# Performance work log

Hardware: AMD Instinct MI355X
Metric: run time of the kernel (lower is better)

## Reference

```python
import jax, jax.numpy as jnp
import numpy as np

EPS = 1e-6
GROUPS = 8


def setup_inputs() -> dict:
    key = jax.random.key(0)
    ks = jax.random.split(key, 8)
    B, C, H, W = 4, 128, 64, 64
    s = 1.0 / np.sqrt(C)
    return {
        "x": jax.random.normal(ks[0], (B, C, H, W), jnp.float32),
        "gn_scale": jnp.ones((C,), jnp.float32),
        "gn_bias": jnp.zeros((C,), jnp.float32),
        "wq": jax.random.normal(ks[1], (C, C), jnp.float32) * s,
        "bq": jnp.zeros((C,), jnp.float32),
        "wk": jax.random.normal(ks[2], (C, C), jnp.float32) * s,
        "bk": jnp.zeros((C,), jnp.float32),
        "wv": jax.random.normal(ks[3], (C, C), jnp.float32) * s,
        "bv": jnp.zeros((C,), jnp.float32),
        "wp": jax.random.normal(ks[4], (C, C), jnp.float32) * s,
        "bp": jnp.zeros((C,), jnp.float32),
    }


def _group_norm(x, scale, bias):
    B, C, H, W = x.shape
    g = x.reshape(B, GROUPS, C // GROUPS, H * W)
    mu = g.mean(axis=(2, 3), keepdims=True)
    var = g.var(axis=(2, 3), keepdims=True)
    g = (g - mu) * jax.lax.rsqrt(var + EPS)
    g = g.reshape(B, C, H, W)
    return g * scale[None, :, None, None] + bias[None, :, None, None]


def reference(x, gn_scale, gn_bias, wq, bq, wk, bk, wv, bv, wp, bp):
    B, C, H, W = x.shape
    N = H * W
    h = _group_norm(x, gn_scale, gn_bias).reshape(B, C, N)
    # 1x1 convs == channel matmuls: (C_out, C_in) x (B, C_in, N)
    q = jnp.einsum('oc,bcn->bon', wq, h) + bq[None, :, None]
    k = jnp.einsum('oc,bcn->bon', wk, h) + bk[None, :, None]
    v = jnp.einsum('oc,bcn->bon', wv, h) + bv[None, :, None]
    # scores: (B, N, N), w[b,n,m] = sum_c q[b,c,n] k[b,c,m]
    w = jnp.einsum('bcn,bcm->bnm', q, k) * (C ** -0.5)
    w = jax.nn.softmax(w, axis=-1)
    # h_[b,c,n] = sum_m w[b,n,m] v[b,c,m]
    h_ = jnp.einsum('bnm,bcm->bcn', w, v)
    out = jnp.einsum('oc,bcn->bon', wp, h_) + bp[None, :, None]
    return x + out.reshape(B, C, H, W)
```

## Files before the change

### kernel.cpp

```cpp
#include <hip/hip_runtime.h>
#include <math.h>

#define B_ 4
#define C_ 128
#define N_ 4096
#define NSPLIT 4
#define MT 32
#define PLD 40
#define HLD 136
#define VTLD 40

typedef float floatx4 __attribute__((ext_vector_type(4)));
typedef short bf16x8 __attribute__((ext_vector_type(8)));

__device__ __forceinline__ ushort f2bf(float f) {
  unsigned u = __float_as_uint(f);
  return (ushort)((u + 0x7FFF + ((u >> 16) & 1)) >> 16);
}
__device__ __forceinline__ float bf2f(ushort u) {
  return __uint_as_float(((unsigned)u) << 16);
}
__device__ __forceinline__ unsigned pkbf(float a, float b) {
  return __builtin_amdgcn_perm(__float_as_uint(a) + 0x8000u,
                               __float_as_uint(b) + 0x8000u, 0x07060302u);
}
__device__ __forceinline__ float fexp2(float x) {
#if __has_builtin(__builtin_amdgcn_exp2f)
  return __builtin_amdgcn_exp2f(x);
#else
  return exp2f(x);
#endif
}
__device__ __forceinline__ void gl2lds16(const ushort* g, ushort* l) {
  __builtin_amdgcn_global_load_lds(
      (const __attribute__((address_space(1))) void*)g,
      (__attribute__((address_space(3))) void*)l, 16, 0, 0);
}

__global__ __launch_bounds__(256) void prep_kernel(
    const float* __restrict__ x, float* __restrict__ gstat,
    const float* __restrict__ wq, const float* __restrict__ wk,
    const float* __restrict__ wv, const float* __restrict__ wp,
    ushort* __restrict__ wB) {
  if (blockIdx.x >= 256) {
    int i = (blockIdx.x - 256) * 256 + threadIdx.x;
    int m = i >> 14, j = i & 16383;
    const float* src = (m == 0) ? wq : (m == 1) ? wk : (m == 2) ? wv : wp;
    wB[i] = f2bf(src[j]);
    return;
  }
  int b = blockIdx.x >> 6, g = (blockIdx.x >> 3) & 7, part = blockIdx.x & 7;
  const float4* xp = (const float4*)(x + (size_t)(b * C_ + g * 16) * N_) + part * 2048;
  float s = 0.f, ss = 0.f;
  for (int i = threadIdx.x; i < 2048; i += 256) {
    float4 v = xp[i];
    s += v.x + v.y + v.z + v.w;
    ss += v.x * v.x + v.y * v.y + v.z * v.z + v.w * v.w;
  }
  #pragma unroll
  for (int o = 32; o > 0; o >>= 1) {
    s += __shfl_down(s, o, 64);
    ss += __shfl_down(ss, o, 64);
  }
  __shared__ float rs[4], rss[4];
  int wid = threadIdx.x >> 6, lane = threadIdx.x & 63;
  if (lane == 0) { rs[wid] = s; rss[wid] = ss; }
  __syncthreads();
  if (threadIdx.x == 0) {
    int slot = (b * 8 + g) * 8 + part;
    gstat[slot]       = rs[0] + rs[1] + rs[2] + rs[3];
    gstat[256 + slot] = rss[0] + rss[1] + rss[2] + rss[3];
  }
}

__global__ __launch_bounds__(256) void gnqkv_kernel(
    const float* __restrict__ x, const float* __restrict__ gstat,
    const float* __restrict__ scale, const float* __restrict__ bias,
    const ushort* __restrict__ wB,
    const float* __restrict__ bq, const float* __restrict__ bk,
    const float* __restrict__ bv,
    ushort* __restrict__ qT, ushort* __restrict__ kT, ushort* __restrict__ vB) {
  __shared__ __align__(16) ushort hs[32][HLD];
  __shared__ __align__(16) ushort Qt[32][HLD];
  __shared__ __align__(16) ushort Kt[32][HLD];
  __shared__ __align__(16) ushort Vt[128][VTLD];
  __shared__ float sSc[C_], sBi[C_];
  int tid = threadIdx.x;
  int b = blockIdx.x >> 7;
  int n0 = (blockIdx.x & 127) * 32;
  if (tid < 128) {
    int g = tid >> 4;
    float S = 0.f, SS = 0.f;
    #pragma unroll
    for (int p = 0; p < 8; ++p) {
      S  += gstat[(b * 8 + g) * 8 + p];
      SS += gstat[256 + (b * 8 + g) * 8 + p];
    }
    float mu = S * (1.f / 65536.f);
    float var = SS * (1.f / 65536.f) - mu * mu;
    float rstd = rsqrtf(var + 1e-6f);
    float sc = scale[tid] * rstd;
    sSc[tid] = sc;
    sBi[tid] = bias[tid] - mu * sc;
  }
  __syncthreads();
  #pragma unroll
  for (int k2 = 0; k2 < 4; ++k2) {
    int i = tid + k2 * 256;
    int c = i >> 3, n4 = i & 7;
    float4 v = *(const float4*)(x + (size_t)(b * C_ + c) * N_ + n0 + n4 * 4);
    float sc = sSc[c], bi = sBi[c];
    hs[n4 * 4 + 0][c] = f2bf(v.x * sc + bi);
    hs[n4 * 4 + 1][c] = f2bf(v.y * sc + bi);
    hs[n4 * 4 + 2][c] = f2bf(v.z * sc + bi);
    hs[n4 * 4 + 3][c] = f2bf(v.w * sc + bi);
  }
  __syncthreads();
  int lane = tid & 63, w = tid >> 6;
  int col = lane & 15, quad = lane >> 4;
  int oh = w * 32;
  bf16x8 hf[2][4];
  #pragma unroll
  for (int nh = 0; nh < 2; ++nh)
    #pragma unroll
    for (int kc = 0; kc < 4; ++kc)
      hf[nh][kc] = *(const bf16x8*)&hs[nh * 16 + col][kc * 32 + quad * 8];
  const ushort* Wq = wB;
  const ushort* Wk = wB + 16384;
  const ushort* Wv = wB + 32768;
  const float scl = 0.12751879752224991f;
  #pragma unroll
  for (int ot = 0; ot < 2; ++ot) {
    int o0 = oh + ot * 16;
    floatx4 aq[2] = {(floatx4)0.f, (floatx4)0.f};
    floatx4 ak[2] = {(floatx4)0.f, (floatx4)0.f};
    floatx4 av[2] = {(floatx4)0.f, (floatx4)0.f};
    #pragma unroll
    for (int kc = 0; kc < 4; ++kc) {
      int wo = (o0 + col) * C_ + kc * 32 + quad * 8;
      bf16x8 wqf = *(const bf16x8*)&Wq[wo];
      bf16x8 wkf = *(const bf16x8*)&Wk[wo];
      bf16x8 wvf = *(const bf16x8*)&Wv[wo];
      #pragma unroll
      for (int nh = 0; nh < 2; ++nh) {
        aq[nh] = __builtin_amdgcn_mfma_f32_16x16x32_bf16(wqf, hf[nh][kc], aq[nh], 0, 0, 0);
        ak[nh] = __builtin_amdgcn_mfma_f32_16x16x32_bf16(wkf, hf[nh][kc], ak[nh], 0, 0, 0);
        av[nh] = __builtin_amdgcn_mfma_f32_16x16x32_bf16(wvf, hf[nh][kc], av[nh], 0, 0, 0);
      }
    }
    float4 bqv = *(const float4*)&bq[o0 + quad * 4];
    float4 bkv = *(const float4*)&bk[o0 + quad * 4];
    float4 bvv = *(const float4*)&bv[o0 + quad * 4];
    #pragma unroll
    for (int nh = 0; nh < 2; ++nh) {
      uint2 qs = { pkbf((aq[nh][1] + bqv.y) * scl, (aq[nh][0] + bqv.x) * scl),
                   pkbf((aq[nh][3] + bqv.w) * scl, (aq[nh][2] + bqv.z) * scl) };
      uint2 ks = { pkbf(ak[nh][1] + bkv.y, ak[nh][0] + bkv.x),
                   pkbf(ak[nh][3] + bkv.w, ak[nh][2] + bkv.z) };
      *(uint2*)&Qt[nh * 16 + col][o0 + quad * 4] = qs;
      *(uint2*)&Kt[nh * 16 + col][o0 + quad * 4] = ks;
      float vv[4] = {av[nh][0] + bvv.x, av[nh][1] + bvv.y,
                     av[nh][2] + bvv.z, av[nh][3] + bvv.w};
      #pragma unroll
      for (int r = 0; r < 4; ++r)
        Vt[o0 + quad * 4 + r][nh * 16 + col] = f2bf(vv[r]);
    }
  }
  __syncthreads();
  #pragma unroll
  for (int rep = 0; rep < 2; ++rep) {
    int idx = tid + rep * 256;
    int row = idx >> 4, seg = idx & 15;
    size_t dst = ((size_t)b * N_ + n0 + row) * C_ + seg * 8;
    *(uint4*)(qT + dst) = *(const uint4*)&Qt[row][seg * 8];
    *(uint4*)(kT + dst) = *(const uint4*)&Kt[row][seg * 8];
  }
  #pragma unroll
  for (int rep = 0; rep < 2; ++rep) {
    int idx = tid + rep * 256;
    int o = idx >> 2, seg = idx & 3;
    *(uint4*)(vB + ((size_t)b * C_ + o) * N_ + n0 + seg * 8) = *(const uint4*)&Vt[o][seg * 8];
  }
}

__global__ __launch_bounds__(512, 4) void attn_kernel(
    const ushort* __restrict__ qT, const ushort* __restrict__ kT,
    const ushort* __restrict__ vB, ushort* __restrict__ Op,
    float* __restrict__ Lv) {
  __shared__ __align__(16) ushort Ks[2][MT * 128];
  __shared__ __align__(16) ushort Vs[2][C_ * MT];
  __shared__ __align__(16) ushort Ps[2][128 * PLD];
  __shared__ float lpart[8][2][16];
  int sp = blockIdx.x & 3;
  int qblk = (blockIdx.x >> 2) & 31;
  int b = blockIdx.x >> 7;
  int n0 = qblk * 128;
  int tid = threadIdx.x, lane = tid & 63, w = tid >> 6;
  int col = lane & 15, quad = lane >> 4;
  int wu = __builtin_amdgcn_readfirstlane(w);
  int mtw = w & 1, qg = w >> 1;
  int qh = w & 1, cq = w >> 1;
  const ushort* kTb = kT + (size_t)b * N_ * C_;
  const ushort* vBb = vB + (size_t)b * C_ * N_;

  bf16x8 qf[2][4];
  #pragma unroll
  for (int qt = 0; qt < 2; ++qt)
    #pragma unroll
    for (int kc = 0; kc < 4; ++kc)
      qf[qt][kc] = *(const bf16x8*)(qT + ((size_t)b * N_ + n0 + qg * 32 + qt * 16 + col) * C_ + kc * 32 + quad * 8);

  floatx4 Oacc[4][2];
  #pragma unroll
  for (int qt = 0; qt < 4; ++qt)
    #pragma unroll
    for (int ct = 0; ct < 2; ++ct) Oacc[qt][ct] = (floatx4)0.f;
  float lacc[2] = {0.f, 0.f};

  const int m00 = sp * 1024;

  const ushort* kgp;
  const ushort* vgp;
  {
    int r = wu * 4 + (lane >> 4);
    int pos = (lane & 15) ^ (r & 7);
    kgp = kTb + (size_t)(m00 + r) * 128 + pos * 8;
    int c = wu * 16 + (lane >> 2);
    int mc = (lane & 3) ^ ((lane >> 3) & 3);
    vgp = vBb + (size_t)c * N_ + m00 + mc * 8;
  }

  #define STAGE(buf)                                   \
    {                                                  \
      gl2lds16(kgp, &Ks[buf][wu * 512]);               \
      gl2lds16(vgp, &Vs[buf][wu * 512]);               \
      kgp += MT * 128;                                 \
      vgp += MT;                                       \
    }

  #define S_COMPUTE(KsB, st)                                                          \
    {                                                                                 \
      int row = mtw * 16 + col;                                                       \
      bf16x8 kf[4];                                                                   \
      _Pragma("unroll")                                                               \
      for (int kc = 0; kc < 4; ++kc)                                                  \
        kf[kc] = *(const bf16x8*)&(KsB)[row * 128 + (((4 * kc + quad) ^ (col & 7)) * 8)]; \
      __builtin_amdgcn_s_setprio(1);                                                  \
      _Pragma("unroll")                                                               \
      for (int qt = 0; qt < 2; ++qt) {                                                \
        floatx4 acc = (floatx4)0.f;                                                   \
        _Pragma("unroll")                                                             \
        for (int kc = 0; kc < 4; ++kc)                                                \
          acc = __builtin_amdgcn_mfma_f32_16x16x32_bf16(kf[kc], qf[qt][kc], acc, 0, 0, 0); \
        st[qt] = acc;                                                                 \
      }                                                                               \
      __builtin_amdgcn_s_setprio(0);                                                  \
    }

  #define SOFTMAX_WRITE(PsB, st)                                                      \
    {                                                                                 \
      _Pragma("unroll")                                                               \
      for (int qt = 0; qt < 2; ++qt) {                                                \
        int prow = (qg * 32 + qt * 16 + col) * PLD + mtw * 16;                        \
        float p0 = fexp2(st[qt][0]);                                                  \
        float p1 = fexp2(st[qt][1]);                                                  \
        float p2 = fexp2(st[qt][2]);                                                  \
        float p3 = fexp2(st[qt][3]);                                                  \
        uint2 pk = { pkbf(p1, p0), pkbf(p3, p2) };                                    \
        *(uint2*)&(PsB)[prow + quad * 4] = pk;                                        \
        lacc[qt] += (p0 + p1) + (p2 + p3);                                            \
      }                                                                               \
    }

  #define V_LOAD(VsB, vfp)                                                            \
    {                                                                                 \
      _Pragma("unroll")                                                               \
      for (int ct = 0; ct < 2; ++ct)                                                  \
        vfp[ct] = *(const bf16x8*)&(VsB)[(cq * 32 + ct * 16 + col) * MT +             \
                                         ((quad ^ ((col >> 1) & 3)) * 8)];            \
    }

  #define PV_COMPUTE(PsB, vfp)                                                        \
    {                                                                                 \
      __builtin_amdgcn_s_setprio(1);                                                  \
      _Pragma("unroll")                                                               \
      for (int qt = 0; qt < 4; ++qt) {                                                \
        bf16x8 pf = *(const bf16x8*)&(PsB)[(qh * 64 + qt * 16 + col) * PLD + quad * 8]; \
        _Pragma("unroll")                                                             \
        for (int ct = 0; ct < 2; ++ct)                                                \
          Oacc[qt][ct] = __builtin_amdgcn_mfma_f32_16x16x32_bf16(pf, vfp[ct], Oacc[qt][ct], 0, 0, 0); \
      }                                                                               \
      __builtin_amdgcn_s_setprio(0);                                                  \
    }

  floatx4 st[2];
  bf16x8 vfp[2];

  STAGE(0);
  __syncthreads();

  STAGE(1);
  S_COMPUTE(Ks[0], st);
  SOFTMAX_WRITE(Ps[0], st);
  V_LOAD(Vs[0], vfp);
  __syncthreads();

  for (int t = 1; t < 31; ++t) {
    STAGE((t + 1) & 1);
    S_COMPUTE(Ks[t & 1], st);
    PV_COMPUTE(Ps[(t - 1) & 1], vfp);
    SOFTMAX_WRITE(Ps[t & 1], st);
    V_LOAD(Vs[t & 1], vfp);
    __syncthreads();
  }

  S_COMPUTE(Ks[1], st);
  PV_COMPUTE(Ps[0], vfp);
  SOFTMAX_WRITE(Ps[1], st);
  V_LOAD(Vs[1], vfp);
  __syncthreads();

  PV_COMPUTE(Ps[1], vfp);

  ushort* OpB = Op + (((size_t)sp * B_ + b) * N_ + n0) * C_;
  #pragma unroll
  for (int qt = 0; qt < 4; ++qt)
    #pragma unroll
    for (int ct = 0; ct < 2; ++ct)
      #pragma unroll
      for (int r = 0; r < 4; ++r)
        OpB[(size_t)(qh * 64 + qt * 16 + quad * 4 + r) * C_ + cq * 32 + ct * 16 + col] =
            f2bf(Oacc[qt][ct][r]);
  #pragma unroll
  for (int qt = 0; qt < 2; ++qt) {
    float lsum = lacc[qt];
    lsum += __shfl_xor(lsum, 16, 64);
    lsum += __shfl_xor(lsum, 32, 64);
    if (quad == 0) lpart[w][qt][col] = lsum;
  }
  __syncthreads();
  if ((w & 1) == 0 && quad == 0) {
    #pragma unroll
    for (int qt = 0; qt < 2; ++qt) {
      int idx = b * N_ + n0 + (w >> 1) * 32 + qt * 16 + col;
      Lv[(size_t)sp * (B_ * N_) + idx] = lpart[w][qt][col] + lpart[w + 1][qt][col];
    }
  }
}

__global__ __launch_bounds__(256) void mergeproj_kernel(
    const ushort* __restrict__ Op, const float* __restrict__ Lv,
    const ushort* __restrict__ wpB, const float* __restrict__ bp,
    const float* __restrict__ x, float* __restrict__ out) {
  __shared__ __align__(16) ushort tile[32 * HLD];
  int tid = threadIdx.x;
  int b = blockIdx.x >> 7;
  int n0 = (blockIdx.x & 127) * 32;
  #pragma unroll
  for (int rep = 0; rep < 2; ++rep) {
    int idx = tid + rep * 256;
    int n = idx >> 4, cc = idx & 15;
    int nIdx = b * N_ + n0 + n;
    float den = Lv[0 * (B_ * N_) + nIdx] + Lv[1 * (B_ * N_) + nIdx] +
                Lv[2 * (B_ * N_) + nIdx] + Lv[3 * (B_ * N_) + nIdx];
    float inv = 1.f / den;
    float o[8];
    #pragma unroll
    for (int j = 0; j < 8; ++j) o[j] = 0.f;
    #pragma unroll
    for (int sp = 0; sp < NSPLIT; ++sp) {
      uint4 d = *(const uint4*)&Op[((size_t)sp * (B_ * N_) + nIdx) * C_ + cc * 8];
      unsigned dd[4] = {d.x, d.y, d.z, d.w};
      #pragma unroll
      for (int j = 0; j < 4; ++j) {
        o[j * 2]     += bf2f((ushort)(dd[j] & 0xFFFF));
        o[j * 2 + 1] += bf2f((ushort)(dd[j] >> 16));
      }
    }
    uint4 res;
    res.x = pkbf(o[1] * inv, o[0] * inv);
    res.y = pkbf(o[3] * inv, o[2] * inv);
    res.z = pkbf(o[5] * inv, o[4] * inv);
    res.w = pkbf(o[7] * inv, o[6] * inv);
    *(uint4*)&tile[n * HLD + cc * 8] = res;
  }
  __syncthreads();
  int lane = tid & 63, w = tid >> 6;
  int col = lane & 15, quad = lane >> 4;
  int oh = w * 32;
  bf16x8 hf[2][4];
  #pragma unroll
  for (int nh = 0; nh < 2; ++nh)
    #pragma unroll
    for (int kc = 0; kc < 4; ++kc)
      hf[nh][kc] = *(const bf16x8*)&tile[(nh * 16 + col) * HLD + kc * 32 + quad * 8];
  #pragma unroll
  for (int ot = 0; ot < 2; ++ot) {
    int o0 = oh + ot * 16;
    floatx4 acc[2] = {(floatx4)0.f, (floatx4)0.f};
    #pragma unroll
    for (int kc = 0; kc < 4; ++kc) {
      int wo = (o0 + col) * C_ + kc * 32 + quad * 8;
      bf16x8 wf = *(const bf16x8*)&wpB[wo];
      #pragma unroll
      for (int nh = 0; nh < 2; ++nh)
        acc[nh] = __builtin_amdgcn_mfma_f32_16x16x32_bf16(wf, hf[nh][kc], acc[nh], 0, 0, 0);
    }
    float4 bpv = *(const float4*)&bp[o0 + quad * 4];
    float bb[4] = {bpv.x, bpv.y, bpv.z, bpv.w};
    #pragma unroll
    for (int nh = 0; nh < 2; ++nh)
      #pragma unroll
      for (int r = 0; r < 4; ++r) {
        size_t idx = ((size_t)b * C_ + o0 + quad * 4 + r) * N_ + n0 + nh * 16 + col;
        out[idx] = acc[nh][r] + bb[r] + x[idx];
      }
  }
}

extern "C" void kernel_launch(void* const* d_in, const int* in_sizes, int n_in,
                              void* d_out, int out_size, void* d_ws, size_t ws_size,
                              hipStream_t stream) {
  const float* x        = (const float*)d_in[0];
  const float* gn_scale = (const float*)d_in[1];
  const float* gn_bias  = (const float*)d_in[2];
  const float* wq = (const float*)d_in[3];
  const float* bq = (const float*)d_in[4];
  const float* wk = (const float*)d_in[5];
  const float* bk = (const float*)d_in[6];
  const float* wv = (const float*)d_in[7];
  const float* bv = (const float*)d_in[8];
  const float* wp = (const float*)d_in[9];
  const float* bp = (const float*)d_in[10];
  float* out = (float*)d_out;

  char* ws = (char*)d_ws;
  float*  Lv    = (float*)(ws + 262144);
  ushort* wB    = (ushort*)(ws + 524288);
  float*  gstat = (float*)(ws + 655360);
  ushort* qT    = (ushort*)(ws + (4u << 20));
  ushort* kT    = (ushort*)(ws + (8u << 20));
  ushort* vB    = (ushort*)(ws + (12u << 20));
  ushort* Op    = (ushort*)(ws + (16u << 20));
  ushort* wpB   = wB + 49152;

  prep_kernel<<<512, 256, 0, stream>>>(x, gstat, wq, wk, wv, wp, wB);
  gnqkv_kernel<<<512, 256, 0, stream>>>(x, gstat, gn_scale, gn_bias, wB, bq, bk, bv, qT, kT, vB);
  attn_kernel<<<512, 512, 0, stream>>>(qT, kT, vB, Op, Lv);
  mergeproj_kernel<<<512, 256, 0, stream>>>(Op, Lv, wpB, bp, x, out);
}
```

Baseline: 142.2 us.

## Fuse four kernels into one persistent kernel with software grid barriers

Merges the prep, groupnorm+QKV, attention and merge+projection kernels into a single 512-block launch of 512 threads. The stages are separated by an atomic-counter grid barrier, and the shared-memory buffers of each stage are aliased onto one raw shared array. This removes three kernel launch gaps and their tail effects, at the cost of a memset launch and spin-wait barriers. It relies on all 512 blocks being co-resident; if they are not, the kernel deadlocks.

```diff
diff --git a/kernel.cpp b/kernel.cpp
--- a/kernel.cpp
+++ b/kernel.cpp
@@ -9,6 +9,7 @@
 #define PLD 40
 #define HLD 136
 #define VTLD 40
+#define NBLK 512u
 
 typedef float floatx4 __attribute__((ext_vector_type(4)));
 typedef short bf16x8 __attribute__((ext_vector_type(8)));
@@ -37,101 +38,123 @@
       (__attribute__((address_space(3))) void*)l, 16, 0, 0);
 }
 
-__global__ __launch_bounds__(256) void prep_kernel(
-    const float* __restrict__ x, float* __restrict__ gstat,
-    const float* __restrict__ wq, const float* __restrict__ wk,
-    const float* __restrict__ wv, const float* __restrict__ wp,
-    ushort* __restrict__ wB) {
-  if (blockIdx.x >= 256) {
-    int i = (blockIdx.x - 256) * 256 + threadIdx.x;
-    int m = i >> 14, j = i & 16383;
-    const float* src = (m == 0) ? wq : (m == 1) ? wk : (m == 2) ? wv : wp;
-    wB[i] = f2bf(src[j]);
-    return;
-  }
-  int b = blockIdx.x >> 6, g = (blockIdx.x >> 3) & 7, part = blockIdx.x & 7;
-  const float4* xp = (const float4*)(x + (size_t)(b * C_ + g * 16) * N_) + part * 2048;
-  float s = 0.f, ss = 0.f;
-  for (int i = threadIdx.x; i < 2048; i += 256) {
-    float4 v = xp[i];
-    s += v.x + v.y + v.z + v.w;
-    ss += v.x * v.x + v.y * v.y + v.z * v.z + v.w * v.w;
-  }
-  #pragma unroll
-  for (int o = 32; o > 0; o >>= 1) {
-    s += __shfl_down(s, o, 64);
-    ss += __shfl_down(ss, o, 64);
-  }
-  __shared__ float rs[4], rss[4];
-  int wid = threadIdx.x >> 6, lane = threadIdx.x & 63;
-  if (lane == 0) { rs[wid] = s; rss[wid] = ss; }
+__device__ __forceinline__ void grid_bar(unsigned* bar) {
   __syncthreads();
   if (threadIdx.x == 0) {
-    int slot = (b * 8 + g) * 8 + part;
-    gstat[slot]       = rs[0] + rs[1] + rs[2] + rs[3];
-    gstat[256 + slot] = rss[0] + rss[1] + rss[2] + rss[3];
-  }
-}
-
-__global__ __launch_bounds__(256) void gnqkv_kernel(
-    const float* __restrict__ x, const float* __restrict__ gstat,
-    const float* __restrict__ scale, const float* __restrict__ bias,
-    const ushort* __restrict__ wB,
-    const float* __restrict__ bq, const float* __restrict__ bk,
-    const float* __restrict__ bv,
-    ushort* __restrict__ qT, ushort* __restrict__ kT, ushort* __restrict__ vB) {
-  __shared__ __align__(16) ushort hs[32][HLD];
-  __shared__ __align__(16) ushort Qt[32][HLD];
-  __shared__ __align__(16) ushort Kt[32][HLD];
-  __shared__ __align__(16) ushort Vt[128][VTLD];
-  __shared__ float sSc[C_], sBi[C_];
-  int tid = threadIdx.x;
-  int b = blockIdx.x >> 7;
-  int n0 = (blockIdx.x & 127) * 32;
-  if (tid < 128) {
-    int g = tid >> 4;
-    float S = 0.f, SS = 0.f;
-    #pragma unroll
-    for (int p = 0; p < 8; ++p) {
-      S  += gstat[(b * 8 + g) * 8 + p];
-      SS += gstat[256 + (b * 8 + g) * 8 + p];
-    }
-    float mu = S * (1.f / 65536.f);
-    float var = SS * (1.f / 65536.f) - mu * mu;
-    float rstd = rsqrtf(var + 1e-6f);
-    float sc = scale[tid] * rstd;
-    sSc[tid] = sc;
-    sBi[tid] = bias[tid] - mu * sc;
+    unsigned gen = __hip_atomic_load(&bar[1], __ATOMIC_RELAXED, __HIP_MEMORY_SCOPE_AGENT);
+    unsigned prev = __hip_atomic_fetch_add(&bar[0], 1u, __ATOMIC_ACQ_REL, __HIP_MEMORY_SCOPE_AGENT);
+    if (prev + 1u == NBLK) {
+      __hip_atomic_store(&bar[0], 0u, __ATOMIC_RELAXED, __HIP_MEMORY_SCOPE_AGENT);
+      __hip_atomic_fetch_add(&bar[1], 1u, __ATOMIC_RELEASE, __HIP_MEMORY_SCOPE_AGENT);
+    } else {
+      while (__hip_atomic_load(&bar[1], __ATOMIC_ACQUIRE, __HIP_MEMORY_SCOPE_AGENT) == gen)
+        __builtin_amdgcn_s_sleep(2);
+    }
   }
   __syncthreads();
-  #pragma unroll
-  for (int k2 = 0; k2 < 4; ++k2) {
-    int i = tid + k2 * 256;
-    int c = i >> 3, n4 = i & 7;
-    float4 v = *(const float4*)(x + (size_t)(b * C_ + c) * N_ + n0 + n4 * 4);
-    float sc = sSc[c], bi = sBi[c];
-    hs[n4 * 4 + 0][c] = f2bf(v.x * sc + bi);
-    hs[n4 * 4 + 1][c] = f2bf(v.y * sc + bi);
-    hs[n4 * 4 + 2][c] = f2bf(v.z * sc + bi);
-    hs[n4 * 4 + 3][c] = f2bf(v.w * sc + bi);
+}
+
+__global__ __launch_bounds__(512, 4) void fused_kernel(
+    const float* __restrict__ x, const float* __restrict__ gn_scale,
+    const float* __restrict__ gn_bias,
+    const float* __restrict__ wq, const float* __restrict__ bq,
+    const float* __restrict__ wk, const float* __restrict__ bk,
+    const float* __restrict__ wv, const float* __restrict__ bv,
+    const float* __restrict__ wp, const float* __restrict__ bp,
+    float* __restrict__ out, unsigned* __restrict__ bar,
+    float* __restrict__ Lv, ushort* __restrict__ wB,
+    float* __restrict__ gstat, ushort* __restrict__ qT, ushort* __restrict__ kT,
+    ushort* __restrict__ vB, ushort* __restrict__ Op) {
+  __shared__ __align__(16) char smem[54272];
+  ushort* sm_u = (ushort*)smem;
+  int bx = blockIdx.x;
+  int tid = threadIdx.x, lane = tid & 63, w = tid >> 6;
+  int col = lane & 15, quad = lane >> 4;
+
+  if (bx >= 256) {
+    if (tid < 256) {
+      int i = (bx - 256) * 256 + tid;
+      int m = i >> 14, j = i & 16383;
+      const float* src = (m == 0) ? wq : (m == 1) ? wk : (m == 2) ? wv : wp;
+      wB[i] = f2bf(src[j]);
+    }
+  } else {
+    int b = bx >> 6, g = (bx >> 3) & 7, part = bx & 7;
+    const float4* xp = (const float4*)(x + (size_t)(b * C_ + g * 16) * N_) + part * 2048;
+    float s = 0.f, ss = 0.f;
+    for (int i = tid; i < 2048; i += 512) {
+      float4 v = xp[i];
+      s += v.x + v.y + v.z + v.w;
+      ss += v.x * v.x + v.y * v.y + v.z * v.z + v.w * v.w;
+    }
+    #pragma unroll
+    for (int o = 32; o > 0; o >>= 1) {
+      s += __shfl_down(s, o, 64);
+      ss += __shfl_down(ss, o, 64);
+    }
+    float* rs = (float*)smem;
+    float* rss = (float*)smem + 8;
+    if (lane == 0) { rs[w] = s; rss[w] = ss; }
+    __syncthreads();
+    if (tid == 0) {
+      float S = 0.f, SS = 0.f;
+      #pragma unroll
+      for (int k = 0; k < 8; ++k) { S += rs[k]; SS += rss[k]; }
+      int slot = (b * 8 + g) * 8 + part;
+      gstat[slot]       = S;
+      gstat[256 + slot] = SS;
+    }
   }
-  __syncthreads();
-  int lane = tid & 63, w = tid >> 6;
-  int col = lane & 15, quad = lane >> 4;
-  int oh = w * 32;
-  bf16x8 hf[2][4];
-  #pragma unroll
-  for (int nh = 0; nh < 2; ++nh)
-    #pragma unroll
-    for (int kc = 0; kc < 4; ++kc)
-      hf[nh][kc] = *(const bf16x8*)&hs[nh * 16 + col][kc * 32 + quad * 8];
-  const ushort* Wq = wB;
-  const ushort* Wk = wB + 16384;
-  const ushort* Wv = wB + 32768;
-  const float scl = 0.12751879752224991f;
-  #pragma unroll
-  for (int ot = 0; ot < 2; ++ot) {
-    int o0 = oh + ot * 16;
+  grid_bar(bar);
+
+  {
+    ushort* hs = sm_u;
+    ushort* Qt = sm_u + 4352;
+    ushort* Kt = sm_u + 8704;
+    ushort* Vt = sm_u + 13056;
+    float* sSc = (float*)(smem + 36352);
+    float* sBi = (float*)(smem + 36864);
+    int b = bx >> 7;
+    int n0 = (bx & 127) * 32;
+    if (tid < 128) {
+      int g = tid >> 4;
+      float S = 0.f, SS = 0.f;
+      #pragma unroll
+      for (int p = 0; p < 8; ++p) {
+        S  += gstat[(b * 8 + g) * 8 + p];
+        SS += gstat[256 + (b * 8 + g) * 8 + p];
+      }
+      float mu = S * (1.f / 65536.f);
+      float var = SS * (1.f / 65536.f) - mu * mu;
+      float rstd = rsqrtf(var + 1e-6f);
+      float sc = gn_scale[tid] * rstd;
+      sSc[tid] = sc;
+      sBi[tid] = gn_bias[tid] - mu * sc;
+    }
+    __syncthreads();
+    #pragma unroll
+    for (int k2 = 0; k2 < 2; ++k2) {
+      int i = tid + k2 * 512;
+      int c = i >> 3, n4 = i & 7;
+      float4 v = *(const float4*)(x + (size_t)(b * C_ + c) * N_ + n0 + n4 * 4);
+      float sc = sSc[c], bi = sBi[c];
+      hs[(n4 * 4 + 0) * HLD + c] = f2bf(v.x * sc + bi);
+      hs[(n4 * 4 + 1) * HLD + c] = f2bf(v.y * sc + bi);
+      hs[(n4 * 4 + 2) * HLD + c] = f2bf(v.z * sc + bi);
+      hs[(n4 * 4 + 3) * HLD + c] = f2bf(v.w * sc + bi);
+    }
+    __syncthreads();
+    int o0 = w * 16;
+    bf16x8 hf[2][4];
+    #pragma unroll
+    for (int nh = 0; nh < 2; ++nh)
+      #pragma unroll
+      for (int kc = 0; kc < 4; ++kc)
+        hf[nh][kc] = *(const bf16x8*)&hs[(nh * 16 + col) * HLD + kc * 32 + quad * 8];
+    const ushort* Wq = wB;
+    const ushort* Wk = wB + 16384;
+    const ushort* Wv = wB + 32768;
+    const float scl = 0.12751879752224991f;
     floatx4 aq[2] = {(floatx4)0.f, (floatx4)0.f};
     floatx4 ak[2] = {(floatx4)0.f, (floatx4)0.f};
     floatx4 av[2] = {(floatx4)0.f, (floatx4)0.f};
@@ -157,246 +180,229 @@
                    pkbf((aq[nh][3] + bqv.w) * scl, (aq[nh][2] + bqv.z) * scl) };
       uint2 ks = { pkbf(ak[nh][1] + bkv.y, ak[nh][0] + bkv.x),
                    pkbf(ak[nh][3] + bkv.w, ak[nh][2] + bkv.z) };
-      *(uint2*)&Qt[nh * 16 + col][o0 + quad * 4] = qs;
-      *(uint2*)&Kt[nh * 16 + col][o0 + quad * 4] = ks;
+      *(uint2*)&Qt[(nh * 16 + col) * HLD + o0 + quad * 4] = qs;
+      *(uint2*)&Kt[(nh * 16 + col) * HLD + o0 + quad * 4] = ks;
       float vv[4] = {av[nh][0] + bvv.x, av[nh][1] + bvv.y,
                      av[nh][2] + bvv.z, av[nh][3] + bvv.w};
       #pragma unroll
       for (int r = 0; r < 4; ++r)
-        Vt[o0 + quad * 4 + r][nh * 16 + col] = f2bf(vv[r]);
+        Vt[(o0 + quad * 4 + r) * VTLD + nh * 16 + col] = f2bf(vv[r]);
+    }
+    __syncthreads();
+    {
+      int row = tid >> 4, seg = tid & 15;
+      size_t dst = ((size_t)b * N_ + n0 + row) * C_ + seg * 8;
+      *(uint4*)(qT + dst) = *(const uint4*)&Qt[row * HLD + seg * 8];
+      *(uint4*)(kT + dst) = *(const uint4*)&Kt[row * HLD + seg * 8];
+    }
+    {
+      int o = tid >> 2, seg = tid & 3;
+      *(uint4*)(vB + ((size_t)b * C_ + o) * N_ + n0 + seg * 8) =
+          *(const uint4*)&Vt[o * VTLD + seg * 8];
     }
   }
-  __syncthreads();
-  #pragma unroll
-  for (int rep = 0; rep < 2; ++rep) {
-    int idx = tid + rep * 256;
-    int row = idx >> 4, seg = idx & 15;
-    size_t dst = ((size_t)b * N_ + n0 + row) * C_ + seg * 8;
-    *(uint4*)(qT + dst) = *(const uint4*)&Qt[row][seg * 8];
-    *(uint4*)(kT + dst) = *(const uint4*)&Kt[row][seg * 8];
+  grid_bar(bar);
+
+  {
+    ushort* Ks = sm_u;
+    ushort* Vs = sm_u + 8192;
+    ushort* Ps = sm_u + 16384;
+    float* lpart = (float*)(smem + 53248);
+    int sp = bx & 3;
+    int qblk = (bx >> 2) & 31;
+    int b = bx >> 7;
+    int n0 = qblk * 128;
+    int wu = __builtin_amdgcn_readfirstlane(w);
+    int mtw = w & 1, qg = w >> 1;
+    int qh = w & 1, cq = w >> 1;
+    const ushort* kTb = kT + (size_t)b * N_ * C_;
+    const ushort* vBb = vB + (size_t)b * C_ * N_;
+
+    bf16x8 qf[2][4];
+    #pragma unroll
+    for (int qt = 0; qt < 2; ++qt)
+      #pragma unroll
+      for (int kc = 0; kc < 4; ++kc)
+        qf[qt][kc] = *(const bf16x8*)(qT + ((size_t)b * N_ + n0 + qg * 32 + qt * 16 + col) * C_ + kc * 32 + quad * 8);
+
+    floatx4 Oacc[4][2];
+    #pragma unroll
+    for (int qt = 0; qt < 4; ++qt)
+      #pragma unroll
+      for (int ct = 0; ct < 2; ++ct) Oacc[qt][ct] = (floatx4)0.f;
+    float lacc[2] = {0.f, 0.f};
+
+    const int m00 = sp * 1024;
+    const ushort* kgp;
+    const ushort* vgp;
+    {
+      int r = wu * 4 + (lane >> 4);
+      int pos = (lane & 15) ^ (r & 7);
+      kgp = kTb + (size_t)(m00 + r) * 128 + pos * 8;
+      int c = wu * 16 + (lane >> 2);
+      int mc = (lane & 3) ^ ((lane >> 3) & 3);
+      vgp = vBb + (size_t)c * N_ + m00 + mc * 8;
+    }
+
+    #define STAGE(buf)                                        \
+      {                                                       \
+        gl2lds16(kgp, Ks + (buf)*4096 + wu * 512);            \
+        gl2lds16(vgp, Vs + (buf)*4096 + wu * 512);            \
+        kgp += MT * 128;                                      \
+        vgp += MT;                                            \
+      }
+
+    #define S_COMPUTE(KsB, st)                                                          \
+      {                                                                                 \
+        int row = mtw * 16 + col;                                                       \
+        bf16x8 kf[4];                                                                   \
+        _Pragma("unroll")                                                               \
+        for (int kc = 0; kc < 4; ++kc)                                                  \
+          kf[kc] = *(const bf16x8*)&(KsB)[row * 128 + (((4 * kc + quad) ^ (col & 7)) * 8)]; \
+        __builtin_amdgcn_s_setprio(1);                                                  \
+        _Pragma("unroll")                                                               \
+        for (int qt = 0; qt < 2; ++qt) {                                                \
+          floatx4 acc = (floatx4)0.f;                                                   \
+          _Pragma("unroll")                                                             \
+          for (int kc = 0; kc < 4; ++kc)                                                \
+            acc = __builtin_amdgcn_mfma_f32_16x16x32_bf16(kf[kc], qf[qt][kc], acc, 0, 0, 0); \
+          st[qt] = acc;                                                                 \
+        }                                                                               \
+        __builtin_amdgcn_s_setprio(0);                                                  \
+      }
+
+    #define SOFTMAX_WRITE(PsB, st)                                                      \
+      {                                                                                 \
+        _Pragma("unroll")                                                               \
+        for (int qt = 0; qt < 2; ++qt) {                                                \
+          int prow = (qg * 32 + qt * 16 + col) * PLD + mtw * 16;                        \
+          float p0 = fexp2(st[qt][0]);                                                  \
+          float p1 = fexp2(st[qt][1]);                                                  \
+          float p2 = fexp2(st[qt][2]);                                                  \
+          float p3 = fexp2(st[qt][3]);                                                  \
+          uint2 pk = { pkbf(p1, p0), pkbf(p3, p2) };                                    \
+          *(uint2*)&(PsB)[prow + quad * 4] = pk;                                        \
+          lacc[qt] += (p0 + p1) + (p2 + p3);                                            \
+        }                                                                               \
+      }
+
+    #define V_LOAD(VsB, vfp)                                                            \
+      {                                                                                 \
+        _Pragma("unroll")                                                               \
+        for (int ct = 0; ct < 2; ++ct)                                                  \
+          vfp[ct] = *(const bf16x8*)&(VsB)[(cq * 32 + ct * 16 + col) * MT +             \
+                                           ((quad ^ ((col >> 1) & 3)) * 8)];            \
+      }
+
+    #define PV_COMPUTE(PsB, vfp)                                                        \
+      {                                                                                 \
+        __builtin_amdgcn_s_setprio(1);                                                  \
+        _Pragma("unroll")                                                               \
+        for (int qt = 0; qt < 4; ++qt) {                                                \
+          bf16x8 pf = *(const bf16x8*)&(PsB)[(qh * 64 + qt * 16 + col) * PLD + quad * 8]; \
+          _Pragma("unroll")                                                             \
+          for (int ct = 0; ct < 2; ++ct)                                                \
+            Oacc[qt][ct] = __builtin_amdgcn_mfma_f32_16x16x32_bf16(pf, vfp[ct], Oacc[qt][ct], 0, 0, 0); \
+        }                                                                               \
+        __builtin_amdgcn_s_setprio(0);                                                  \
+      }
+
+    floatx4 st[2];
+    bf16x8 vfp[2];
+
+    STAGE(0);
+    __syncthreads();
+
+    STAGE(1);
+    S_COMPUTE(Ks, st);
+    SOFTMAX_WRITE(Ps, st);
+    V_LOAD(Vs, vfp);
+    __syncthreads();
+
+    for (int t = 1; t < 31; ++t) {
+      STAGE((t + 1) & 1);
+      S_COMPUTE(Ks + (t & 1) * 4096, st);
+      PV_COMPUTE(Ps + ((t - 1) & 1) * 5120, vfp);
+      SOFTMAX_WRITE(Ps + (t & 1) * 5120, st);
+      V_LOAD(Vs + (t & 1) * 4096, vfp);
+      __syncthreads();
+    }
+
+    S_COMPUTE(Ks + 4096, st);
+    PV_COMPUTE(Ps, vfp);
+    SOFTMAX_WRITE(Ps + 5120, st);
+    V_LOAD(Vs + 4096, vfp);
+    __syncthreads();
+
+    PV_COMPUTE(Ps + 5120, vfp);
+
+    ushort* OpB = Op + (((size_t)sp * B_ + b) * N_ + n0) * C_;
+    #pragma unroll
+    for (int qt = 0; qt < 4; ++qt)
+      #pragma unroll
+      for (int ct = 0; ct < 2; ++ct)
+        #pragma unroll
+        for (int r = 0; r < 4; ++r)
+          OpB[(size_t)(qh * 64 + qt * 16 + quad * 4 + r) * C_ + cq * 32 + ct * 16 + col] =
+              f2bf(Oacc[qt][ct][r]);
+    #pragma unroll
+    for (int qt = 0; qt < 2; ++qt) {
+      float lsum = lacc[qt];
+      lsum += __shfl_xor(lsum, 16, 64);
+      lsum += __shfl_xor(lsum, 32, 64);
+      if (quad == 0) lpart[(w * 2 + qt) * 16 + col] = lsum;
+    }
+    __syncthreads();
+    if ((w & 1) == 0 && quad == 0) {
+      #pragma unroll
+      for (int qt = 0; qt < 2; ++qt) {
+        int idx = b * N_ + n0 + (w >> 1) * 32 + qt * 16 + col;
+        Lv[(size_t)sp * (B_ * N_) + idx] =
+            lpart[(w * 2 + qt) * 16 + col] + lpart[((w + 1) * 2 + qt) * 16 + col];
+      }
+    }
   }
-  #pragma unroll
-  for (int rep = 0; rep < 2; ++rep) {
-    int idx = tid + rep * 256;
-    int o = idx >> 2, seg = idx & 3;
-    *(uint4*)(vB + ((size_t)b * C_ + o) * N_ + n0 + seg * 8) = *(const uint4*)&Vt[o][seg * 8];
-  }
-}
-
-__global__ __launch_bounds__(512, 4) void attn_kernel(
-    const ushort* __restrict__ qT, const ushort* __restrict__ kT,
-    const ushort* __restrict__ vB, ushort* __restrict__ Op,
-    float* __restrict__ Lv) {
-  __shared__ __align__(16) ushort Ks[2][MT * 128];
-  __shared__ __align__(16) ushort Vs[2][C_ * MT];
-  __shared__ __align__(16) ushort Ps[2][128 * PLD];
-  __shared__ float lpart[8][2][16];
-  int sp = blockIdx.x & 3;
-  int qblk = (blockIdx.x >> 2) & 31;
-  int b = blockIdx.x >> 7;
-  int n0 = qblk * 128;
-  int tid = threadIdx.x, lane = tid & 63, w = tid >> 6;
-  int col = lane & 15, quad = lane >> 4;
-  int wu = __builtin_amdgcn_readfirstlane(w);
-  int mtw = w & 1, qg = w >> 1;
-  int qh = w & 1, cq = w >> 1;
-  const ushort* kTb = kT + (size_t)b * N_ * C_;
-  const ushort* vBb = vB + (size_t)b * C_ * N_;
-
-  bf16x8 qf[2][4];
-  #pragma unroll
-  for (int qt = 0; qt < 2; ++qt)
-    #pragma unroll
-    for (int kc = 0; kc < 4; ++kc)
-      qf[qt][kc] = *(const bf16x8*)(qT + ((size_t)b * N_ + n0 + qg * 32 + qt * 16 + col) * C_ + kc * 32 + quad * 8);
-
-  floatx4 Oacc[4][2];
-  #pragma unroll
-  for (int qt = 0; qt < 4; ++qt)
-    #pragma unroll
-    for (int ct = 0; ct < 2; ++ct) Oacc[qt][ct] = (floatx4)0.f;
-  float lacc[2] = {0.f, 0.f};
-
-  const int m00 = sp * 1024;
-
-  const ushort* kgp;
-  const ushort* vgp;
+  grid_bar(bar);
+
   {
-    int r = wu * 4 + (lane >> 4);
-    int pos = (lane & 15) ^ (r & 7);
-    kgp = kTb + (size_t)(m00 + r) * 128 + pos * 8;
-    int c = wu * 16 + (lane >> 2);
-    int mc = (lane & 3) ^ ((lane >> 3) & 3);
-    vgp = vBb + (size_t)c * N_ + m00 + mc * 8;
-  }
-
-  #define STAGE(buf)                                   \
-    {                                                  \
-      gl2lds16(kgp, &Ks[buf][wu * 512]);               \
-      gl2lds16(vgp, &Vs[buf][wu * 512]);               \
-      kgp += MT * 128;                                 \
-      vgp += MT;                                       \
-    }
-
-  #define S_COMPUTE(KsB, st)                                                          \
-    {                                                                                 \
-      int row = mtw * 16 + col;                                                       \
-      bf16x8 kf[4];                                                                   \
-      _Pragma("unroll")                                                               \
-      for (int kc = 0; kc < 4; ++kc)                                                  \
-        kf[kc] = *(const bf16x8*)&(KsB)[row * 128 + (((4 * kc + quad) ^ (col & 7)) * 8)]; \
-      __builtin_amdgcn_s_setprio(1);                                                  \
-      _Pragma("unroll")                                                               \
-      for (int qt = 0; qt < 2; ++qt) {                                                \
-        floatx4 acc = (floatx4)0.f;                                                   \
-        _Pragma("unroll")                                                             \
-        for (int kc = 0; kc < 4; ++kc)                                                \
-          acc = __builtin_amdgcn_mfma_f32_16x16x32_bf16(kf[kc], qf[qt][kc], acc, 0, 0, 0); \
-        st[qt] = acc;                                                                 \
-      }                                                                               \
-      __builtin_amdgcn_s_setprio(0);                                                  \
-    }
-
-  #define SOFTMAX_WRITE(PsB, st)                                                      \
-    {                                                                                 \
-      _Pragma("unroll")                                                               \
-      for (int qt = 0; qt < 2; ++qt) {                                                \
-        int prow = (qg * 32 + qt * 16 + col) * PLD + mtw * 16;                        \
-        float p0 = fexp2(st[qt][0]);                                                  \
-        float p1 = fexp2(st[qt][1]);                                                  \
-        float p2 = fexp2(st[qt][2]);                                                  \
-        float p3 = fexp2(st[qt][3]);                                                  \
-        uint2 pk = { pkbf(p1, p0), pkbf(p3, p2) };                                    \
-        *(uint2*)&(PsB)[prow + quad * 4] = pk;                                        \
-        lacc[qt] += (p0 + p1) + (p2 + p3);                                            \
-      }                                                                               \
-    }
-
-  #define V_LOAD(VsB, vfp)                                                            \
-    {                                                                                 \
-      _Pragma("unroll")                                                               \
-      for (int ct = 0; ct < 2; ++ct)                                                  \
-        vfp[ct] = *(const bf16x8*)&(VsB)[(cq * 32 + ct * 16 + col) * MT +             \
-                                         ((quad ^ ((col >> 1) & 3)) * 8)];            \
-    }
-
-  #define PV_COMPUTE(PsB, vfp)                                                        \
-    {                                                                                 \
-      __builtin_amdgcn_s_setprio(1);                                                  \
-      _Pragma("unroll")                                                               \
-      for (int qt = 0; qt < 4; ++qt) {                                                \
-        bf16x8 pf = *(const bf16x8*)&(PsB)[(qh * 64 + qt * 16 + col) * PLD + quad * 8]; \
-        _Pragma("unroll")                                                             \
-        for (int ct = 0; ct < 2; ++ct)                                                \
-          Oacc[qt][ct] = __builtin_amdgcn_mfma_f32_16x16x32_bf16(pf, vfp[ct], Oacc[qt][ct], 0, 0, 0); \
-      }                                                                               \
-      __builtin_amdgcn_s_setprio(0);                                                  \
-    }
-
-  floatx4 st[2];
-  bf16x8 vfp[2];
-
-  STAGE(0);
-  __syncthreads();
-
-  STAGE(1);
-  S_COMPUTE(Ks[0], st);
-  SOFTMAX_WRITE(Ps[0], st);
-  V_LOAD(Vs[0], vfp);
-  __syncthreads();
-
-  for (int t = 1; t < 31; ++t) {
-    STAGE((t + 1) & 1);
-    S_COMPUTE(Ks[t & 1], st);
-    PV_COMPUTE(Ps[(t - 1) & 1], vfp);
-    SOFTMAX_WRITE(Ps[t & 1], st);
-    V_LOAD(Vs[t & 1], vfp);
-    __syncthreads();
-  }
-
-  S_COMPUTE(Ks[1], st);
-  PV_COMPUTE(Ps[0], vfp);
-  SOFTMAX_WRITE(Ps[1], st);
-  V_LOAD(Vs[1], vfp);
-  __syncthreads();
-
-  PV_COMPUTE(Ps[1], vfp);
-
-  ushort* OpB = Op + (((size_t)sp * B_ + b) * N_ + n0) * C_;
-  #pragma unroll
-  for (int qt = 0; qt < 4; ++qt)
-    #pragma unroll
-    for (int ct = 0; ct < 2; ++ct)
-      #pragma unroll
-      for (int r = 0; r < 4; ++r)
-        OpB[(size_t)(qh * 64 + qt * 16 + quad * 4 + r) * C_ + cq * 32 + ct * 16 + col] =
-            f2bf(Oacc[qt][ct][r]);
-  #pragma unroll
-  for (int qt = 0; qt < 2; ++qt) {
-    float lsum = lacc[qt];
-    lsum += __shfl_xor(lsum, 16, 64);
-    lsum += __shfl_xor(lsum, 32, 64);
-    if (quad == 0) lpart[w][qt][col] = lsum;
-  }
-  __syncthreads();
-  if ((w & 1) == 0 && quad == 0) {
-    #pragma unroll
-    for (int qt = 0; qt < 2; ++qt) {
-      int idx = b * N_ + n0 + (w >> 1) * 32 + qt * 16 + col;
-      Lv[(size_t)sp * (B_ * N_) + idx] = lpart[w][qt][col] + lpart[w + 1][qt][col];
-    }
-  }
-}
-
-__global__ __launch_bounds__(256) void mergeproj_kernel(
-    const ushort* __restrict__ Op, const float* __restrict__ Lv,
-    const ushort* __restrict__ wpB, const float* __restrict__ bp,
-    const float* __restrict__ x, float* __restrict__ out) {
-  __shared__ __align__(16) ushort tile[32 * HLD];
-  int tid = threadIdx.x;
-  int b = blockIdx.x >> 7;
-  int n0 = (blockIdx.x & 127) * 32;
-  #pragma unroll
-  for (int rep = 0; rep < 2; ++rep) {
-    int idx = tid + rep * 256;
-    int n = idx >> 4, cc = idx & 15;
-    int nIdx = b * N_ + n0 + n;
-    float den = Lv[0 * (B_ * N_) + nIdx] + Lv[1 * (B_ * N_) + nIdx] +
-                Lv[2 * (B_ * N_) + nIdx] + Lv[3 * (B_ * N_) + nIdx];
-    float inv = 1.f / den;
-    float o[8];
-    #pragma unroll
-    for (int j = 0; j < 8; ++j) o[j] = 0.f;
-    #pragma unroll
-    for (int sp = 0; sp < NSPLIT; ++sp) {
-      uint4 d = *(const uint4*)&Op[((size_t)sp * (B_ * N_) + nIdx) * C_ + cc * 8];
-      unsigned dd[4] = {d.x, d.y, d.z, d.w};
-      #pragma unroll
-      for (int j = 0; j < 4; ++j) {
-        o[j * 2]     += bf2f((ushort)(dd[j] & 0xFFFF));
-        o[j * 2 + 1] += bf2f((ushort)(dd[j] >> 16));
-      }
-    }
-    uint4 res;
-    res.x = pkbf(o[1] * inv, o[0] * inv);
-    res.y = pkbf(o[3] * inv, o[2] * inv);
-    res.z = pkbf(o[5] * inv, o[4] * inv);
-    res.w = pkbf(o[7] * inv, o[6] * inv);
-    *(uint4*)&tile[n * HLD + cc * 8] = res;
-  }
-  __syncthreads();
-  int lane = tid & 63, w = tid >> 6;
-  int col = lane & 15, quad = lane >> 4;
-  int oh = w * 32;
-  bf16x8 hf[2][4];
-  #pragma unroll
-  for (int nh = 0; nh < 2; ++nh)
-    #pragma unroll
-    for (int kc = 0; kc < 4; ++kc)
-      hf[nh][kc] = *(const bf16x8*)&tile[(nh * 16 + col) * HLD + kc * 32 + quad * 8];
-  #pragma unroll
-  for (int ot = 0; ot < 2; ++ot) {
-    int o0 = oh + ot * 16;
+    ushort* tile = sm_u;
+    const ushort* wpB = wB + 49152;
+    int b = bx >> 7;
+    int n0 = (bx & 127) * 32;
+    {
+      int n = tid >> 4, cc = tid & 15;
+      int nIdx = b * N_ + n0 + n;
+      float den = Lv[0 * (B_ * N_) + nIdx] + Lv[1 * (B_ * N_) + nIdx] +
+                  Lv[2 * (B_ * N_) + nIdx] + Lv[3 * (B_ * N_) + nIdx];
+      float inv = 1.f / den;
+      float o[8];
+      #pragma unroll
+      for (int j = 0; j < 8; ++j) o[j] = 0.f;
+      #pragma unroll
+      for (int sp = 0; sp < NSPLIT; ++sp) {
+        uint4 d = *(const uint4*)&Op[((size_t)sp * (B_ * N_) + nIdx) * C_ + cc * 8];
+        unsigned dd[4] = {d.x, d.y, d.z, d.w};
+        #pragma unroll
+        for (int j = 0; j < 4; ++j) {
+          o[j * 2]     += bf2f((ushort)(dd[j] & 0xFFFF));
+          o[j * 2 + 1] += bf2f((ushort)(dd[j] >> 16));
+        }
+      }
+      uint4 res;
+      res.x = pkbf(o[1] * inv, o[0] * inv);
+      res.y = pkbf(o[3] * inv, o[2] * inv);
+      res.z = pkbf(o[5] * inv, o[4] * inv);
+      res.w = pkbf(o[7] * inv, o[6] * inv);
+      *(uint4*)&tile[n * HLD + cc * 8] = res;
+    }
+    __syncthreads();
+    int o0 = w * 16;
+    bf16x8 hf[2][4];
+    #pragma unroll
+    for (int nh = 0; nh < 2; ++nh)
+      #pragma unroll
+      for (int kc = 0; kc < 4; ++kc)
+        hf[nh][kc] = *(const bf16x8*)&tile[(nh * 16 + col) * HLD + kc * 32 + quad * 8];
     floatx4 acc[2] = {(floatx4)0.f, (floatx4)0.f};
     #pragma unroll
     for (int kc = 0; kc < 4; ++kc) {
@@ -435,6 +441,7 @@
   float* out = (float*)d_out;
 
   char* ws = (char*)d_ws;
+  unsigned* bar = (unsigned*)ws;
   float*  Lv    = (float*)(ws + 262144);
   ushort* wB    = (ushort*)(ws + 524288);
   float*  gstat = (float*)(ws + 655360);
@@ -442,10 +449,9 @@
   ushort* kT    = (ushort*)(ws + (8u << 20));
   ushort* vB    = (ushort*)(ws + (12u << 20));
   ushort* Op    = (ushort*)(ws + (16u << 20));
-  ushort* wpB   = wB + 49152;
-
-  prep_kernel<<<512, 256, 0, stream>>>(x, gstat, wq, wk, wv, wp, wB);
-  gnqkv_kernel<<<512, 256, 0, stream>>>(x, gstat, gn_scale, gn_bias, wB, bq, bk, bv, qT, kT, vB);
-  attn_kernel<<<512, 512, 0, stream>>>(qT, kT, vB, Op, Lv);
-  mergeproj_kernel<<<512, 256, 0, stream>>>(Op, Lv, wpB, bp, x, out);
-}
+
+  hipMemsetAsync(bar, 0, 64, stream);
+  fused_kernel<<<512, 512, 0, stream>>>(x, gn_scale, gn_bias, wq, bq, wk, bk,
+                                        wv, bv, wp, bp, out, bar, Lv, wB, gstat,
+                                        qT, kT, vB, Op);
+}
```

Measured after the change: 363.8 us. 2.56x slower.
